# Kernel tuning notes

Measured on AMD Instinct MI355X. Metric: run time of the kernel, lower is better.

Reference implementation:

```python
import jax, jax.numpy as jnp
import numpy as np

N = 10000          # num nodes
E = 640000         # num edges (avg degree 64)
IN_CH = 128
OUT_CH = 128


def setup_inputs() -> dict:
    key = jax.random.key(0)
    k_x, k_ei, k_ea, k_w1, k_b1, k_w2, k_b2 = jax.random.split(key, 7)
    x = jax.random.normal(k_x, (N, IN_CH), dtype=jnp.float32)
    edge_index = jax.random.randint(k_ei, (2, E), 0, N, dtype=jnp.int64)
    edge_attr = jax.random.uniform(k_ea, (E,), dtype=jnp.float32)
    # MLP params: Linear(2*in, out) -> ReLU -> Linear(out, out), stored as [in, out]
    s1 = 1.0 / np.sqrt(2 * IN_CH)
    s2 = 1.0 / np.sqrt(OUT_CH)
    W1 = jax.random.uniform(k_w1, (2 * IN_CH, OUT_CH), jnp.float32, -s1, s1)
    b1 = jax.random.uniform(k_b1, (OUT_CH,), jnp.float32, -s1, s1)
    W2 = jax.random.uniform(k_w2, (OUT_CH, OUT_CH), jnp.float32, -s2, s2)
    b2 = jax.random.uniform(k_b2, (OUT_CH,), jnp.float32, -s2, s2)
    return {"x": x, "edge_index": edge_index, "edge_attr": edge_attr,
            "W1": W1, "b1": b1, "W2": W2, "b2": b2}


def reference(x, edge_index, edge_attr, W1, b1, W2, b2):
    row, col = edge_index[0], edge_index[1]
    # message: scale sender feature by edge_attr, concat with receiver feature, 2-layer MLP
    x_i = x[row] * edge_attr[:, None]          # [E, in]
    x_j = x[col]                               # [E, in]
    combined = jnp.concatenate([x_i, x_j], axis=1)  # [E, 2*in]
    h = jax.nn.relu(combined @ W1 + b1)        # [E, out]
    messages = h @ W2 + b2                     # [E, out]
    # sum aggregation: scatter-add messages into receiving nodes (col)
    out = jnp.zeros((x.shape[0], messages.shape[1]), dtype=messages.dtype)
    out = out.at[col].add(messages)
    return out
```

## Files before the change

### kernel.cpp

```cpp
#include <hip/hip_runtime.h>

#define C 128
#define NPB 16
#define CAP 128
#define OVF_MAX 65536
#define EPT1 16
#define GSH 5
#define G (1 << GSH)
#define CAPB 3072
#define MAXBIN 512

__device__ __forceinline__ unsigned bf16_bits(float x) {
    unsigned u = __float_as_uint(x);
    u += 0x7FFFu + ((u >> 16) & 1u);
    return u >> 16;
}

__global__ void fused_pre_kernel(const float* __restrict__ x, const float* __restrict__ W1,
                                 unsigned short* __restrict__ P16, float* __restrict__ Q,
                                 const int* __restrict__ ei, const float* __restrict__ attr,
                                 uint2* __restrict__ bins, int* __restrict__ bin_cursor,
                                 int* __restrict__ ovf_cnt, int2* __restrict__ ovf,
                                 int N, int E, int PBLK, int NBIN) {
    if ((int)blockIdx.x < PBLK) {
        __shared__ int hist[MAXBIN];
        __shared__ int boff[MAXBIN];
        for (int i = threadIdx.x; i < NBIN; i += 256) { hist[i] = 0; boff[i] = 0; }
        __syncthreads();
        const int base = ((int)blockIdx.x * 256 + (int)threadIdx.x) * EPT1;
        const int rem = (base < E) ? min(EPT1, E - base) : 0;
        const bool vec = (rem == EPT1) && ((E & 3) == 0);
        if (vec) {
#pragma unroll
            for (int j0 = 0; j0 < EPT1; j0 += 4) {
                const int4 c = *(const int4*)(ei + (size_t)E + base + j0);
                atomicAdd(&hist[c.x >> GSH], 1);
                atomicAdd(&hist[c.y >> GSH], 1);
                atomicAdd(&hist[c.z >> GSH], 1);
                atomicAdd(&hist[c.w >> GSH], 1);
            }
        } else {
            for (int j = 0; j < rem; ++j)
                atomicAdd(&hist[ei[(size_t)E + base + j] >> GSH], 1);
        }
        __syncthreads();
        for (int i = threadIdx.x; i < NBIN; i += 256) {
            const int c = hist[i];
            int b = 0;
            if (c) {
                const int cp = (c + 7) & ~7;
                b = atomicAdd(&bin_cursor[i], cp);
                for (int k = c; k < cp; ++k)
                    if (b + k < CAPB)
                        bins[(size_t)i * CAPB + b + k] = make_uint2(0u, 0xFFFFFFFFu);
            }
            hist[i] = b;
        }
        __syncthreads();
        if (vec) {
#pragma unroll
            for (int j0 = 0; j0 < EPT1; j0 += 4) {
                const int4 r = *(const int4*)(ei + base + j0);
                const int4 c = *(const int4*)(ei + (size_t)E + base + j0);
                const float4 a = *(const float4*)(attr + base + j0);
                const int rr[4] = {r.x, r.y, r.z, r.w};
                const int cc[4] = {c.x, c.y, c.z, c.w};
                const float aa[4] = {a.x, a.y, a.z, a.w};
#pragma unroll
                for (int j = 0; j < 4; ++j) {
                    const int bin = cc[j] >> GSH;
                    const int idx = hist[bin] + atomicAdd(&boff[bin], 1);
                    const unsigned pk = (bf16_bits(aa[j]) << 16) | (unsigned)rr[j];
                    if (idx < CAPB) {
                        bins[(size_t)bin * CAPB + idx] = make_uint2(pk, (unsigned)cc[j]);
                    } else {
                        const int o = atomicAdd(ovf_cnt, 1);
                        if (o < OVF_MAX) ovf[o] = make_int2(cc[j], (int)pk);
                    }
                }
            }
        } else {
            for (int j = 0; j < rem; ++j) {
                const int row = ei[base + j], colv = ei[(size_t)E + base + j];
                const int bin = colv >> GSH;
                const int idx = hist[bin] + atomicAdd(&boff[bin], 1);
                const unsigned pk = (bf16_bits(attr[base + j]) << 16) | (unsigned)row;
                if (idx < CAPB) {
                    bins[(size_t)bin * CAPB + idx] = make_uint2(pk, (unsigned)colv);
                } else {
                    const int o = atomicAdd(ovf_cnt, 1);
                    if (o < OVF_MAX) ovf[o] = make_int2(colv, (int)pk);
                }
            }
        }
    } else {
        __shared__ float xs[NPB][C];
        const int pb = (int)blockIdx.x - PBLK;
        const int n0 = pb * NPB;
        const int tt = threadIdx.x & (C - 1);
        const int half = threadIdx.x >> 7;
        for (int i = threadIdx.x; i < NPB * C; i += 256) {
            const int gi = n0 * C + i;
            xs[0][i] = (gi < N * C) ? x[gi] : 0.f;
        }
        __syncthreads();
        const float* __restrict__ Wb = W1 + (half ? (C * C) : 0) + tt;
        float acc[NPB] = {};
        for (int k = 0; k < C; ++k) {
            const float w = Wb[k * C];
#pragma unroll
            for (int j = 0; j < NPB; ++j)
                acc[j] = fmaf(xs[j][k], w, acc[j]);
        }
#pragma unroll
        for (int j = 0; j < NPB; ++j)
            if (n0 + j < N) {
                if (half) Q[(size_t)(n0 + j) * C + tt] = acc[j];
                else      P16[(size_t)(n0 + j) * C + tt] = (unsigned short)bf16_bits(acc[j]);
            }
    }
}

__global__ void bin_scatter_kernel(const uint2* __restrict__ bins, const int* __restrict__ bin_cursor,
                                   unsigned* __restrict__ sorted, int* __restrict__ cursor,
                                   int* __restrict__ ovf_cnt, int2* __restrict__ ovf, int N) {
    __shared__ int off[G];
    const int b = blockIdx.x;
    const int n0 = b << GSH;
    if (threadIdx.x < G) off[threadIdx.x] = 0;
    __syncthreads();
    const int cnt = min(bin_cursor[b], CAPB);
    const uint2* __restrict__ src = bins + (size_t)b * CAPB;
    for (int i = threadIdx.x; i < cnt; i += 256) {
        const uint2 e = src[i];
        const unsigned noff = e.y - (unsigned)n0;
        if (noff < (unsigned)G) {
            const int pos = atomicAdd(&off[noff], 1);
            if (pos < CAP) {
                sorted[(size_t)e.y * CAP + pos] = e.x;
            } else {
                const int o = atomicAdd(ovf_cnt, 1);
                if (o < OVF_MAX) ovf[o] = make_int2((int)e.y, (int)e.x);
            }
        }
    }
    __syncthreads();
    if (threadIdx.x < G && n0 + (int)threadIdx.x < N)
        cursor[n0 + threadIdx.x] = min(off[threadIdx.x], CAP);
}

__global__ void agg_kernel(const unsigned* __restrict__ sorted, const int* __restrict__ cursor,
                           const unsigned short* __restrict__ P16, const float* __restrict__ Q,
                           const float* __restrict__ b1,
                           const int* __restrict__ ovf_cnt, const int2* __restrict__ ovf,
                           float* __restrict__ H, int* __restrict__ degw, int N) {
    __shared__ unsigned ebuf[2][CAP];
    __shared__ float4 red[2][8][32];
    const int t = threadIdx.x;
    const int j = t >> 7;
    const int tl = t & 127;
    const int grp = tl >> 4;
    const int ch8 = t & 15;
    const int n = blockIdx.x * 2 + j;

    int deg = 0, cnt = 0, mcnt = 0;
    if (n < N) {
        deg = cursor[n];
        cnt = min(deg, CAP);
        for (int i = tl; i < cnt; i += 128)
            ebuf[j][i] = sorted[(size_t)n * CAP + i];
    }
    __syncthreads();

    float4 acc0 = make_float4(0.f, 0.f, 0.f, 0.f);
    float4 acc1 = acc0;
    if (n < N) {
        const float4 qlo = *(const float4*)(Q + (size_t)n * C + (ch8 << 3));
        const float4 qhi = *(const float4*)(Q + (size_t)n * C + (ch8 << 3) + 4);
        const float4 blo = *(const float4*)(b1 + (ch8 << 3));
        const float4 bhi = *(const float4*)(b1 + (ch8 << 3) + 4);
        const float4 qb0 = make_float4(qlo.x + blo.x, qlo.y + blo.y, qlo.z + blo.z, qlo.w + blo.w);
        const float4 qb1 = make_float4(qhi.x + bhi.x, qhi.y + bhi.y, qhi.z + bhi.z, qhi.w + bhi.w);
        const int chunk = (cnt + 7) >> 3;
        const int s0 = min(grp * chunk, cnt);
        const int s1 = min(s0 + chunk, cnt);
        int i = s0;
        for (; i + 2 <= s1; i += 2) {
            const unsigned e0 = ebuf[j][i], e1 = ebuf[j][i + 1];
            const uint4 p0 = *(const uint4*)(P16 + (((size_t)(e0 & 0xFFFFu)) << 7) + (ch8 << 3));
            const uint4 p1 = *(const uint4*)(P16 + (((size_t)(e1 & 0xFFFFu)) << 7) + (ch8 << 3));
            const float a0 = __uint_as_float(e0 & 0xFFFF0000u);
            const float a1 = __uint_as_float(e1 & 0xFFFF0000u);
            acc0.x += fmaxf(fmaf(a0, __uint_as_float(p0.x << 16),         qb0.x), 0.f)
                    + fmaxf(fmaf(a1, __uint_as_float(p1.x << 16),         qb0.x), 0.f);
            acc0.y += fmaxf(fmaf(a0, __uint_as_float(p0.x & 0xFFFF0000u), qb0.y), 0.f)
                    + fmaxf(fmaf(a1, __uint_as_float(p1.x & 0xFFFF0000u), qb0.y), 0.f);
            acc0.z += fmaxf(fmaf(a0, __uint_as_float(p0.y << 16),         qb0.z), 0.f)
                    + fmaxf(fmaf(a1, __uint_as_float(p1.y << 16),         qb0.z), 0.f);
            acc0.w += fmaxf(fmaf(a0, __uint_as_float(p0.y & 0xFFFF0000u), qb0.w), 0.f)
                    + fmaxf(fmaf(a1, __uint_as_float(p1.y & 0xFFFF0000u), qb0.w), 0.f);
            acc1.x += fmaxf(fmaf(a0, __uint_as_float(p0.z << 16),         qb1.x), 0.f)
                    + fmaxf(fmaf(a1, __uint_as_float(p1.z << 16),         qb1.x), 0.f);
            acc1.y += fmaxf(fmaf(a0, __uint_as_float(p0.z & 0xFFFF0000u), qb1.y), 0.f)
                    + fmaxf(fmaf(a1, __uint_as_float(p1.z & 0xFFFF0000u), qb1.y), 0.f);
            acc1.z += fmaxf(fmaf(a0, __uint_as_float(p0.w << 16),         qb1.z), 0.f)
                    + fmaxf(fmaf(a1, __uint_as_float(p1.w << 16),         qb1.z), 0.f);
            acc1.w += fmaxf(fmaf(a0, __uint_as_float(p0.w & 0xFFFF0000u), qb1.w), 0.f)
                    + fmaxf(fmaf(a1, __uint_as_float(p1.w & 0xFFFF0000u), qb1.w), 0.f);
        }
        for (; i < s1; ++i) {
            const unsigned e0 = ebuf[j][i];
            const uint4 p0 = *(const uint4*)(P16 + (((size_t)(e0 & 0xFFFFu)) << 7) + (ch8 << 3));
            const float a0 = __uint_as_float(e0 & 0xFFFF0000u);
            acc0.x += fmaxf(fmaf(a0, __uint_as_float(p0.x << 16),         qb0.x), 0.f);
            acc0.y += fmaxf(fmaf(a0, __uint_as_float(p0.x & 0xFFFF0000u), qb0.y), 0.f);
            acc0.z += fmaxf(fmaf(a0, __uint_as_float(p0.y << 16),         qb0.z), 0.f);
            acc0.w += fmaxf(fmaf(a0, __uint_as_float(p0.y & 0xFFFF0000u), qb0.w), 0.f);
            acc1.x += fmaxf(fmaf(a0, __uint_as_float(p0.z << 16),         qb1.x), 0.f);
            acc1.y += fmaxf(fmaf(a0, __uint_as_float(p0.z & 0xFFFF0000u), qb1.y), 0.f);
            acc1.z += fmaxf(fmaf(a0, __uint_as_float(p0.w << 16),         qb1.z), 0.f);
            acc1.w += fmaxf(fmaf(a0, __uint_as_float(p0.w & 0xFFFF0000u), qb1.w), 0.f);
        }
        if (grp == 0) {
            const int oc = min(*ovf_cnt, OVF_MAX);
            for (int o = 0; o < oc; ++o) {
                const int2 v = ovf[o];
                if (v.x == n) {
                    ++mcnt;
                    const unsigned u = (unsigned)v.y;
                    const uint4 p0 = *(const uint4*)(P16 + (((size_t)(u & 0xFFFFu)) << 7) + (ch8 << 3));
                    const float a0 = __uint_as_float(u & 0xFFFF0000u);
                    acc0.x += fmaxf(fmaf(a0, __uint_as_float(p0.x << 16),         qb0.x), 0.f);
                    acc0.y += fmaxf(fmaf(a0, __uint_as_float(p0.x & 0xFFFF0000u), qb0.y), 0.f);
                    acc0.z += fmaxf(fmaf(a0, __uint_as_float(p0.y << 16),         qb0.z), 0.f);
                    acc0.w += fmaxf(fmaf(a0, __uint_as_float(p0.y & 0xFFFF0000u), qb0.w), 0.f);
                    acc1.x += fmaxf(fmaf(a0, __uint_as_float(p0.z << 16),         qb1.x), 0.f);
                    acc1.y += fmaxf(fmaf(a0, __uint_as_float(p0.z & 0xFFFF0000u), qb1.y), 0.f);
                    acc1.z += fmaxf(fmaf(a0, __uint_as_float(p0.w << 16),         qb1.z), 0.f);
                    acc1.w += fmaxf(fmaf(a0, __uint_as_float(p0.w & 0xFFFF0000u), qb1.w), 0.f);
                }
            }
        }
    }
    red[j][grp][(ch8 << 1)]     = acc0;
    red[j][grp][(ch8 << 1) | 1] = acc1;
    __syncthreads();
    if (n < N) {
        if (tl == 0) degw[n] = deg + mcnt;
        if (tl < 32) {
            float4 s = red[j][0][tl];
#pragma unroll
            for (int g = 1; g < 8; ++g) {
                const float4 r = red[j][g][tl];
                s.x += r.x; s.y += r.y; s.z += r.z; s.w += r.w;
            }
            *(float4*)(H + (size_t)n * C + (tl << 2)) = s;
        }
    }
}

__global__ void out_gemm_kernel(const float* __restrict__ H, const float* __restrict__ W2,
                                const float* __restrict__ b2, const int* __restrict__ degw,
                                float* __restrict__ out, int N) {
    __shared__ float hsm[NPB][C];
    const int n0 = (int)blockIdx.x * NPB;
    const int col = threadIdx.x & (C - 1);
    const int half = threadIdx.x >> 7;
    for (int i = threadIdx.x; i < NPB * C; i += 256) {
        const int gi = n0 * C + i;
        hsm[0][i] = (gi < N * C) ? H[gi] : 0.f;
    }
    __syncthreads();
    float acc[8] = {};
    for (int k = 0; k < C; ++k) {
        const float w = W2[k * C + col];
#pragma unroll
        for (int j = 0; j < 8; ++j)
            acc[j] = fmaf(hsm[half * 8 + j][k], w, acc[j]);
    }
    const float bv = b2[col];
#pragma unroll
    for (int j = 0; j < 8; ++j) {
        const int n = n0 + half * 8 + j;
        if (n < N) out[(size_t)n * C + col] = fmaf((float)degw[n], bv, acc[j]);
    }
}

extern "C" void kernel_launch(void* const* d_in, const int* in_sizes, int n_in,
                              void* d_out, int out_size, void* d_ws, size_t ws_size,
                              hipStream_t stream) {
    const float* x    = (const float*)d_in[0];
    const int*   ei   = (const int*)d_in[1];
    const float* attr = (const float*)d_in[2];
    const float* W1   = (const float*)d_in[3];
    const float* b1   = (const float*)d_in[4];
    const float* W2   = (const float*)d_in[5];
    const float* b2   = (const float*)d_in[6];
    float* out = (float*)d_out;

    const int N = in_sizes[0] / C;
    const int E = in_sizes[2];
    const int NBIN = (N + G - 1) >> GSH;

    char* ws = (char*)d_ws;
    unsigned short* P16 = (unsigned short*)ws;  ws += (size_t)N * C * sizeof(unsigned short);
    ws = (char*)(((uintptr_t)ws + 15) & ~(uintptr_t)15);
    float*    Q       = (float*)ws;     ws += (size_t)N * C * sizeof(float);
    float*    H       = (float*)ws;     ws += (size_t)N * C * sizeof(float);
    unsigned* sorted  = (unsigned*)ws;  ws += (size_t)N * CAP * sizeof(unsigned);
    uint2*    bins    = (uint2*)ws;     ws += (size_t)NBIN * CAPB * sizeof(uint2);
    int2*     ovf     = (int2*)ws;      ws += (size_t)OVF_MAX * sizeof(int2);
    int*      cursor  = (int*)ws;       ws += (size_t)N * sizeof(int);
    int*      degw    = (int*)ws;       ws += (size_t)N * sizeof(int);
    int*      bin_cursor = (int*)ws;    ws += (size_t)NBIN * sizeof(int);
    int*      ovf_cnt = (int*)ws;

    hipMemsetAsync(bin_cursor, 0, ((size_t)NBIN + 1) * sizeof(int), stream);

    const int PBLK = (E + 256 * EPT1 - 1) / (256 * EPT1);
    const int PB = (N + NPB - 1) / NPB;
    fused_pre_kernel<<<PBLK + PB, 256, 0, stream>>>(x, W1, P16, Q, ei, attr,
                                                    bins, bin_cursor, ovf_cnt, ovf,
                                                    N, E, PBLK, NBIN);
    bin_scatter_kernel<<<NBIN, 256, 0, stream>>>(bins, bin_cursor, sorted, cursor,
                                                 ovf_cnt, ovf, N);
    agg_kernel<<<(N + 1) / 2, 256, 0, stream>>>(sorted, cursor, P16, Q, b1,
                                                ovf_cnt, ovf, H, degw, N);
    out_gemm_kernel<<<(N + NPB - 1) / NPB, 256, 0, stream>>>(H, W2, b2, degw, out, N);
}
```

Measured before the change: 137.3 us.

## Fuse bin scatter, edge aggregation and output GEMM into one per-bin kernel

Bin scatter, the per-node edge aggregation and the W2 output GEMM are merged into a single kernel that works on one 16-node bin. Sorted edge lists, the aggregated H rows and the degrees stay in shared memory rather than going through global buffers, which also drops two kernel launches. To support this the bin width is halved, edges per pre-kernel thread are doubled, and bin cursors are spaced apart to reduce atomic contention. The risk is parallelism: each node's edges are now processed by only 16 threads, and the grid is much smaller than the old aggregation grid, so gather latency may be less well hidden.

```diff
diff --git a/kernel.cpp b/kernel.cpp
--- a/kernel.cpp
+++ b/kernel.cpp
@@ -4,11 +4,12 @@
 #define NPB 16
 #define CAP 128
 #define OVF_MAX 65536
-#define EPT1 16
-#define GSH 5
+#define EPT1 32
+#define GSH 4
 #define G (1 << GSH)
-#define CAPB 3072
-#define MAXBIN 512
+#define CAPB 1792
+#define MAXBIN 1024
+#define BCS 16
 
 __device__ __forceinline__ unsigned bf16_bits(float x) {
     unsigned u = __float_as_uint(x);
@@ -49,7 +50,7 @@
             int b = 0;
             if (c) {
                 const int cp = (c + 7) & ~7;
-                b = atomicAdd(&bin_cursor[i], cp);
+                b = atomicAdd(&bin_cursor[i * BCS], cp);
                 for (int k = c; k < cp; ++k)
                     if (b + k < CAPB)
                         bins[(size_t)i * CAPB + b + k] = make_uint2(0u, 0xFFFFFFFFu);
@@ -121,23 +122,29 @@
     }
 }
 
-__global__ void bin_scatter_kernel(const uint2* __restrict__ bins, const int* __restrict__ bin_cursor,
-                                   unsigned* __restrict__ sorted, int* __restrict__ cursor,
-                                   int* __restrict__ ovf_cnt, int2* __restrict__ ovf, int N) {
+__global__ void bin_agg_out_kernel(const uint2* __restrict__ bins, const int* __restrict__ bin_cursor,
+                                   const unsigned short* __restrict__ P16, const float* __restrict__ Q,
+                                   const float* __restrict__ b1, const float* __restrict__ W2,
+                                   const float* __restrict__ b2,
+                                   int* __restrict__ ovf_cnt, int2* __restrict__ ovf,
+                                   float* __restrict__ out, int N) {
+    __shared__ unsigned smem[G][C];
     __shared__ int off[G];
+    float* __restrict__ smemf = (float*)&smem[0][0];
+    const int t = threadIdx.x;
     const int b = blockIdx.x;
     const int n0 = b << GSH;
-    if (threadIdx.x < G) off[threadIdx.x] = 0;
+    if (t < G) off[t] = 0;
     __syncthreads();
-    const int cnt = min(bin_cursor[b], CAPB);
+    const int cnt = min(bin_cursor[b * BCS], CAPB);
     const uint2* __restrict__ src = bins + (size_t)b * CAPB;
-    for (int i = threadIdx.x; i < cnt; i += 256) {
+    for (int i = t; i < cnt; i += 256) {
         const uint2 e = src[i];
         const unsigned noff = e.y - (unsigned)n0;
         if (noff < (unsigned)G) {
             const int pos = atomicAdd(&off[noff], 1);
             if (pos < CAP) {
-                sorted[(size_t)e.y * CAP + pos] = e.x;
+                smem[noff][pos] = e.x;
             } else {
                 const int o = atomicAdd(ovf_cnt, 1);
                 if (o < OVF_MAX) ovf[o] = make_int2((int)e.y, (int)e.x);
@@ -145,144 +152,84 @@
         }
     }
     __syncthreads();
-    if (threadIdx.x < G && n0 + (int)threadIdx.x < N)
-        cursor[n0 + threadIdx.x] = min(off[threadIdx.x], CAP);
-}
-
-__global__ void agg_kernel(const unsigned* __restrict__ sorted, const int* __restrict__ cursor,
-                           const unsigned short* __restrict__ P16, const float* __restrict__ Q,
-                           const float* __restrict__ b1,
-                           const int* __restrict__ ovf_cnt, const int2* __restrict__ ovf,
-                           float* __restrict__ H, int* __restrict__ degw, int N) {
-    __shared__ unsigned ebuf[2][CAP];
-    __shared__ float4 red[2][8][32];
-    const int t = threadIdx.x;
-    const int j = t >> 7;
-    const int tl = t & 127;
-    const int grp = tl >> 4;
+    const int g = t >> 4;
     const int ch8 = t & 15;
-    const int n = blockIdx.x * 2 + j;
-
-    int deg = 0, cnt = 0, mcnt = 0;
-    if (n < N) {
-        deg = cursor[n];
-        cnt = min(deg, CAP);
-        for (int i = tl; i < cnt; i += 128)
-            ebuf[j][i] = sorted[(size_t)n * CAP + i];
-    }
-    __syncthreads();
-
+    const int n = n0 + g;
+#define PROC(ew, p, qb0, qb1)                                                            \
+    {                                                                                    \
+        const float a_ = __uint_as_float((ew) & 0xFFFF0000u);                            \
+        acc0.x += fmaxf(fmaf(a_, __uint_as_float((p).x << 16),         qb0.x), 0.f);     \
+        acc0.y += fmaxf(fmaf(a_, __uint_as_float((p).x & 0xFFFF0000u), qb0.y), 0.f);     \
+        acc0.z += fmaxf(fmaf(a_, __uint_as_float((p).y << 16),         qb0.z), 0.f);     \
+        acc0.w += fmaxf(fmaf(a_, __uint_as_float((p).y & 0xFFFF0000u), qb0.w), 0.f);     \
+        acc1.x += fmaxf(fmaf(a_, __uint_as_float((p).z << 16),         qb1.x), 0.f);     \
+        acc1.y += fmaxf(fmaf(a_, __uint_as_float((p).z & 0xFFFF0000u), qb1.y), 0.f);     \
+        acc1.z += fmaxf(fmaf(a_, __uint_as_float((p).w << 16),         qb1.z), 0.f);     \
+        acc1.w += fmaxf(fmaf(a_, __uint_as_float((p).w & 0xFFFF0000u), qb1.w), 0.f);     \
+    }
     float4 acc0 = make_float4(0.f, 0.f, 0.f, 0.f);
     float4 acc1 = acc0;
+    int degp = 0, mcnt = 0;
     if (n < N) {
+        degp = min(off[g], CAP);
         const float4 qlo = *(const float4*)(Q + (size_t)n * C + (ch8 << 3));
         const float4 qhi = *(const float4*)(Q + (size_t)n * C + (ch8 << 3) + 4);
         const float4 blo = *(const float4*)(b1 + (ch8 << 3));
         const float4 bhi = *(const float4*)(b1 + (ch8 << 3) + 4);
         const float4 qb0 = make_float4(qlo.x + blo.x, qlo.y + blo.y, qlo.z + blo.z, qlo.w + blo.w);
         const float4 qb1 = make_float4(qhi.x + bhi.x, qhi.y + bhi.y, qhi.z + bhi.z, qhi.w + bhi.w);
-        const int chunk = (cnt + 7) >> 3;
-        const int s0 = min(grp * chunk, cnt);
-        const int s1 = min(s0 + chunk, cnt);
-        int i = s0;
-        for (; i + 2 <= s1; i += 2) {
-            const unsigned e0 = ebuf[j][i], e1 = ebuf[j][i + 1];
-            const uint4 p0 = *(const uint4*)(P16 + (((size_t)(e0 & 0xFFFFu)) << 7) + (ch8 << 3));
-            const uint4 p1 = *(const uint4*)(P16 + (((size_t)(e1 & 0xFFFFu)) << 7) + (ch8 << 3));
-            const float a0 = __uint_as_float(e0 & 0xFFFF0000u);
-            const float a1 = __uint_as_float(e1 & 0xFFFF0000u);
-            acc0.x += fmaxf(fmaf(a0, __uint_as_float(p0.x << 16),         qb0.x), 0.f)
-                    + fmaxf(fmaf(a1, __uint_as_float(p1.x << 16),         qb0.x), 0.f);
-            acc0.y += fmaxf(fmaf(a0, __uint_as_float(p0.x & 0xFFFF0000u), qb0.y), 0.f)
-                    + fmaxf(fmaf(a1, __uint_as_float(p1.x & 0xFFFF0000u), qb0.y), 0.f);
-            acc0.z += fmaxf(fmaf(a0, __uint_as_float(p0.y << 16),         qb0.z), 0.f)
-                    + fmaxf(fmaf(a1, __uint_as_float(p1.y << 16),         qb0.z), 0.f);
-            acc0.w += fmaxf(fmaf(a0, __uint_as_float(p0.y & 0xFFFF0000u), qb0.w), 0.f)
-                    + fmaxf(fmaf(a1, __uint_as_float(p1.y & 0xFFFF0000u), qb0.w), 0.f);
-            acc1.x += fmaxf(fmaf(a0, __uint_as_float(p0.z << 16),         qb1.x), 0.f)
-                    + fmaxf(fmaf(a1, __uint_as_float(p1.z << 16),         qb1.x), 0.f);
-            acc1.y += fmaxf(fmaf(a0, __uint_as_float(p0.z & 0xFFFF0000u), qb1.y), 0.f)
-                    + fmaxf(fmaf(a1, __uint_as_float(p1.z & 0xFFFF0000u), qb1.y), 0.f);
-            acc1.z += fmaxf(fmaf(a0, __uint_as_float(p0.w << 16),         qb1.z), 0.f)
-                    + fmaxf(fmaf(a1, __uint_as_float(p1.w << 16),         qb1.z), 0.f);
-            acc1.w += fmaxf(fmaf(a0, __uint_as_float(p0.w & 0xFFFF0000u), qb1.w), 0.f)
-                    + fmaxf(fmaf(a1, __uint_as_float(p1.w & 0xFFFF0000u), qb1.w), 0.f);
-        }
-        for (; i < s1; ++i) {
-            const unsigned e0 = ebuf[j][i];
-            const uint4 p0 = *(const uint4*)(P16 + (((size_t)(e0 & 0xFFFFu)) << 7) + (ch8 << 3));
-            const float a0 = __uint_as_float(e0 & 0xFFFF0000u);
-            acc0.x += fmaxf(fmaf(a0, __uint_as_float(p0.x << 16),         qb0.x), 0.f);
-            acc0.y += fmaxf(fmaf(a0, __uint_as_float(p0.x & 0xFFFF0000u), qb0.y), 0.f);
-            acc0.z += fmaxf(fmaf(a0, __uint_as_float(p0.y << 16),         qb0.z), 0.f);
-            acc0.w += fmaxf(fmaf(a0, __uint_as_float(p0.y & 0xFFFF0000u), qb0.w), 0.f);
-            acc1.x += fmaxf(fmaf(a0, __uint_as_float(p0.z << 16),         qb1.x), 0.f);
-            acc1.y += fmaxf(fmaf(a0, __uint_as_float(p0.z & 0xFFFF0000u), qb1.y), 0.f);
-            acc1.z += fmaxf(fmaf(a0, __uint_as_float(p0.w << 16),         qb1.z), 0.f);
-            acc1.w += fmaxf(fmaf(a0, __uint_as_float(p0.w & 0xFFFF0000u), qb1.w), 0.f);
-        }
-        if (grp == 0) {
-            const int oc = min(*ovf_cnt, OVF_MAX);
-            for (int o = 0; o < oc; ++o) {
-                const int2 v = ovf[o];
-                if (v.x == n) {
-                    ++mcnt;
-                    const unsigned u = (unsigned)v.y;
-                    const uint4 p0 = *(const uint4*)(P16 + (((size_t)(u & 0xFFFFu)) << 7) + (ch8 << 3));
-                    const float a0 = __uint_as_float(u & 0xFFFF0000u);
-                    acc0.x += fmaxf(fmaf(a0, __uint_as_float(p0.x << 16),         qb0.x), 0.f);
-                    acc0.y += fmaxf(fmaf(a0, __uint_as_float(p0.x & 0xFFFF0000u), qb0.y), 0.f);
-                    acc0.z += fmaxf(fmaf(a0, __uint_as_float(p0.y << 16),         qb0.z), 0.f);
-                    acc0.w += fmaxf(fmaf(a0, __uint_as_float(p0.y & 0xFFFF0000u), qb0.w), 0.f);
-                    acc1.x += fmaxf(fmaf(a0, __uint_as_float(p0.z << 16),         qb1.x), 0.f);
-                    acc1.y += fmaxf(fmaf(a0, __uint_as_float(p0.z & 0xFFFF0000u), qb1.y), 0.f);
-                    acc1.z += fmaxf(fmaf(a0, __uint_as_float(p0.w << 16),         qb1.z), 0.f);
-                    acc1.w += fmaxf(fmaf(a0, __uint_as_float(p0.w & 0xFFFF0000u), qb1.w), 0.f);
-                }
-            }
-        }
-    }
-    red[j][grp][(ch8 << 1)]     = acc0;
-    red[j][grp][(ch8 << 1) | 1] = acc1;
+        int i = 0;
+        for (; i + 4 <= degp; i += 4) {
+            const uint4 e4 = *(const uint4*)(&smem[g][i]);
+            const uint4 p0 = *(const uint4*)(P16 + (((size_t)(e4.x & 0xFFFFu)) << 7) + (ch8 << 3));
+            const uint4 p1 = *(const uint4*)(P16 + (((size_t)(e4.y & 0xFFFFu)) << 7) + (ch8 << 3));
+            const uint4 p2 = *(const uint4*)(P16 + (((size_t)(e4.z & 0xFFFFu)) << 7) + (ch8 << 3));
+            const uint4 p3 = *(const uint4*)(P16 + (((size_t)(e4.w & 0xFFFFu)) << 7) + (ch8 << 3));
+            PROC(e4.x, p0, qb0, qb1);
+            PROC(e4.y, p1, qb0, qb1);
+            PROC(e4.z, p2, qb0, qb1);
+            PROC(e4.w, p3, qb0, qb1);
+        }
+        for (; i < degp; ++i) {
+            const unsigned ew = smem[g][i];
+            const uint4 p = *(const uint4*)(P16 + (((size_t)(ew & 0xFFFFu)) << 7) + (ch8 << 3));
+            PROC(ew, p, qb0, qb1);
+        }
+        const int oc = min(*ovf_cnt, OVF_MAX);
+        for (int o = 0; o < oc; ++o) {
+            const int2 v = ovf[o];
+            if (v.x == n) {
+                ++mcnt;
+                const unsigned ew = (unsigned)v.y;
+                const uint4 p = *(const uint4*)(P16 + (((size_t)(ew & 0xFFFFu)) << 7) + (ch8 << 3));
+                PROC(ew, p, qb0, qb1);
+            }
+        }
+        *(float4*)(smemf + g * C + (ch8 << 3))     = acc0;
+        *(float4*)(smemf + g * C + (ch8 << 3) + 4) = acc1;
+        if (ch8 == 0) off[g] = degp + mcnt;
+    }
+#undef PROC
     __syncthreads();
-    if (n < N) {
-        if (tl == 0) degw[n] = deg + mcnt;
-        if (tl < 32) {
-            float4 s = red[j][0][tl];
-#pragma unroll
-            for (int g = 1; g < 8; ++g) {
-                const float4 r = red[j][g][tl];
-                s.x += r.x; s.y += r.y; s.z += r.z; s.w += r.w;
-            }
-            *(float4*)(H + (size_t)n * C + (tl << 2)) = s;
-        }
-    }
-}
-
-__global__ void out_gemm_kernel(const float* __restrict__ H, const float* __restrict__ W2,
-                                const float* __restrict__ b2, const int* __restrict__ degw,
-                                float* __restrict__ out, int N) {
-    __shared__ float hsm[NPB][C];
-    const int n0 = (int)blockIdx.x * NPB;
-    const int col = threadIdx.x & (C - 1);
-    const int half = threadIdx.x >> 7;
-    for (int i = threadIdx.x; i < NPB * C; i += 256) {
-        const int gi = n0 * C + i;
-        hsm[0][i] = (gi < N * C) ? H[gi] : 0.f;
-    }
-    __syncthreads();
+    const int col = t & (C - 1);
+    const int half = t >> 7;
     float acc[8] = {};
-    for (int k = 0; k < C; ++k) {
-        const float w = W2[k * C + col];
-#pragma unroll
-        for (int j = 0; j < 8; ++j)
-            acc[j] = fmaf(hsm[half * 8 + j][k], w, acc[j]);
+    for (int k = 0; k < C; k += 4) {
+        const float w0 = W2[(k + 0) * C + col];
+        const float w1 = W2[(k + 1) * C + col];
+        const float w2v = W2[(k + 2) * C + col];
+        const float w3 = W2[(k + 3) * C + col];
+#pragma unroll
+        for (int j = 0; j < 8; ++j) {
+            const float4 h4 = *(const float4*)(smemf + (half * 8 + j) * C + k);
+            acc[j] = fmaf(h4.x, w0, fmaf(h4.y, w1, fmaf(h4.z, w2v, fmaf(h4.w, w3, acc[j]))));
+        }
     }
     const float bv = b2[col];
 #pragma unroll
     for (int j = 0; j < 8; ++j) {
-        const int n = n0 + half * 8 + j;
-        if (n < N) out[(size_t)n * C + col] = fmaf((float)degw[n], bv, acc[j]);
+        const int n2 = n0 + half * 8 + j;
+        if (n2 < N) out[(size_t)n2 * C + col] = fmaf((float)off[half * 8 + j], bv, acc[j]);
     }
 }
 
@@ -306,25 +253,18 @@
     unsigned short* P16 = (unsigned short*)ws;  ws += (size_t)N * C * sizeof(unsigned short);
     ws = (char*)(((uintptr_t)ws + 15) & ~(uintptr_t)15);
     float*    Q       = (float*)ws;     ws += (size_t)N * C * sizeof(float);
-    float*    H       = (float*)ws;     ws += (size_t)N * C * sizeof(float);
-    unsigned* sorted  = (unsigned*)ws;  ws += (size_t)N * CAP * sizeof(unsigned);
     uint2*    bins    = (uint2*)ws;     ws += (size_t)NBIN * CAPB * sizeof(uint2);
     int2*     ovf     = (int2*)ws;      ws += (size_t)OVF_MAX * sizeof(int2);
-    int*      cursor  = (int*)ws;       ws += (size_t)N * sizeof(int);
-    int*      degw    = (int*)ws;       ws += (size_t)N * sizeof(int);
-    int*      bin_cursor = (int*)ws;    ws += (size_t)NBIN * sizeof(int);
+    int*      bin_cursor = (int*)ws;    ws += (size_t)NBIN * BCS * sizeof(int);
     int*      ovf_cnt = (int*)ws;
 
-    hipMemsetAsync(bin_cursor, 0, ((size_t)NBIN + 1) * sizeof(int), stream);
+    hipMemsetAsync(bin_cursor, 0, ((size_t)NBIN * BCS + 1) * sizeof(int), stream);
 
     const int PBLK = (E + 256 * EPT1 - 1) / (256 * EPT1);
     const int PB = (N + NPB - 1) / NPB;
     fused_pre_kernel<<<PBLK + PB, 256, 0, stream>>>(x, W1, P16, Q, ei, attr,
                                                     bins, bin_cursor, ovf_cnt, ovf,
                                                     N, E, PBLK, NBIN);
-    bin_scatter_kernel<<<NBIN, 256, 0, stream>>>(bins, bin_cursor, sorted, cursor,
-                                                 ovf_cnt, ovf, N);
-    agg_kernel<<<(N + 1) / 2, 256, 0, stream>>>(sorted, cursor, P16, Q, b1,
-                                                ovf_cnt, ovf, H, degw, N);
-    out_gemm_kernel<<<(N + NPB - 1) / NPB, 256, 0, stream>>>(H, W2, b2, degw, out, N);
-}
+    bin_agg_out_kernel<<<NBIN, 256, 0, stream>>>(bins, bin_cursor, P16, Q, b1, W2, b2,
+                                                 ovf_cnt, ovf, out, N);
+}
```

New measurement: 131.8 us. 1.04x faster.
